# Kernel tuning notes

Measured on AMD Instinct MI355X. Metric: run time of the kernel, lower is better.

Reference implementation:

```python
import jax, jax.numpy as jnp
import numpy as np

EMBED = 1024
HEADS = 16
HEAD_DIM = EMBED // HEADS


def setup_inputs() -> dict:
    key = jax.random.key(0)
    ks = jax.random.split(key, 8)
    N, L = 2, 2048
    values = jax.random.normal(ks[0], (N, L, EMBED), dtype=jnp.float32)
    keys_ = jax.random.normal(ks[1], (N, L, EMBED), dtype=jnp.float32)
    query = jax.random.normal(ks[2], (N, L, EMBED), dtype=jnp.float32)
    mask = jnp.ones((N, 1, 1, L), dtype=jnp.int32)
    s = 1.0 / np.sqrt(EMBED)
    W_q = jax.random.normal(ks[3], (EMBED, EMBED), dtype=jnp.float32) * s
    W_k = jax.random.normal(ks[4], (EMBED, EMBED), dtype=jnp.float32) * s
    W_v = jax.random.normal(ks[5], (EMBED, EMBED), dtype=jnp.float32) * s
    W_o = jax.random.normal(ks[6], (EMBED, EMBED), dtype=jnp.float32) * s
    b_o = jax.random.normal(ks[7], (EMBED,), dtype=jnp.float32) * 0.01
    return {"values": values, "keys": keys_, "query": query, "mask": mask,
            "W_q": W_q, "W_k": W_k, "W_v": W_v, "W_o": W_o, "b_o": b_o}


def reference(values, keys, query, mask, W_q, W_k, W_v, W_o, b_o):
    N, Lq, _ = query.shape
    Lk = keys.shape[1]
    # projections (torch Linear: x @ W.T); reshape to (N, H, L, Dh)
    q = (query @ W_q.T).reshape(N, Lq, HEADS, HEAD_DIM).transpose(0, 2, 1, 3)
    k = (keys @ W_k.T).reshape(N, Lk, HEADS, HEAD_DIM).transpose(0, 2, 1, 3)
    v = (values @ W_v.T).reshape(N, Lk, HEADS, HEAD_DIM).transpose(0, 2, 1, 3)
    energy = jnp.einsum('bhqd,bhkd->bhqk', q, k) / jnp.sqrt(jnp.float32(HEAD_DIM))
    energy = jnp.where(mask == 0, jnp.float32(-1e20), energy)
    attn = jax.nn.softmax(energy, axis=-1)
    out = jnp.einsum('bhqk,bhkd->bhqd', attn, v)
    out = out.transpose(0, 2, 1, 3).reshape(N, Lq, EMBED)
    return out @ W_o.T + b_o
```

## Files before the change

### kernel.cpp

```cpp
#include <hip/hip_runtime.h>
#include <cstddef>
#include <cstdint>

#define SEQ    2048
#define NBATCH 2

typedef unsigned short u16;
typedef unsigned int   u32;
typedef __attribute__((ext_vector_type(8))) short bf16x8;
typedef __attribute__((ext_vector_type(4))) float f32x4;

#if __has_builtin(__builtin_amdgcn_exp2f)
#define EXP2F(x) __builtin_amdgcn_exp2f(x)
#else
#define EXP2F(x) exp2f(x)
#endif

__device__ __forceinline__ u32 fbits(float x) { union { float f; u32 u; } c; c.f = x; return c.u; }
__device__ __forceinline__ u16 f2bf(float x) { return (u16)((fbits(x) + 0x8000u) >> 16); }
__device__ __forceinline__ u32 pack2bf(float lo, float hi) {
    return __builtin_amdgcn_perm(fbits(hi) + 0x8000u, fbits(lo) + 0x8000u, 0x07060302u);
}

__global__ __launch_bounds__(256)
void cast_all(const float* __restrict__ q, const float* __restrict__ k, const float* __restrict__ v,
              const float* __restrict__ wq, const float* __restrict__ wk,
              const float* __restrict__ wv, const float* __restrict__ wo,
              u16* __restrict__ oq, u16* __restrict__ ok, u16* __restrict__ ov,
              u16* __restrict__ owq, u16* __restrict__ owk, u16* __restrict__ owv,
              u16* __restrict__ owo)
{
    const float* s; u16* d; int i;
    if (blockIdx.y == 0)      { s = q; d = oq; i = blockIdx.x * 256 + threadIdx.x; }
    else if (blockIdx.y == 1) { s = k; d = ok; i = blockIdx.x * 256 + threadIdx.x; }
    else if (blockIdx.y == 2) { s = v; d = ov; i = blockIdx.x * 256 + threadIdx.x; }
    else {
        const int w = blockIdx.x >> 10, xi = blockIdx.x & 1023;
        if (w == 0)      { s = wq; d = owq; }
        else if (w == 1) { s = wk; d = owk; }
        else if (w == 2) { s = wv; d = owv; }
        else             { s = wo; d = owo; }
        i = xi * 256 + threadIdx.x;
    }
    float4 vv = ((const float4*)s)[i];
    uint2 r; r.x = pack2bf(vv.x, vv.y); r.y = pack2bf(vv.z, vv.w);
    ((uint2*)d)[i] = r;
}

__device__ __forceinline__
void gemm_body(const u16* __restrict__ X, const u16* __restrict__ W,
               void* __restrict__ Yv, const int layout)
{
    __shared__ u16 smem[2 * 128 * 72];
    u16* As = smem;
    u16* Bs = smem + 128 * 72;

    const int tid  = threadIdx.x;
    const int wave = tid >> 6;
    const int lane = tid & 63;
    const int lm   = lane & 15;
    const int quad = lane >> 4;
    const int m0 = blockIdx.x * 128;
    const int n0 = blockIdx.y * 128;
    const int wr = (wave & 1) * 64;
    const int wc = (wave >> 1) * 64;

    const int srow = tid >> 1;
    const int scol = (tid & 1) * 32;
    const u16* xg = X + (size_t)(m0 + srow) * 1024 + scol;
    const u16* wg = W + (size_t)(n0 + srow) * 1024 + scol;

    bf16x8 pa[4], pb[4];
    #pragma unroll
    for (int p = 0; p < 4; ++p) {
        pa[p] = *(const bf16x8*)(xg + p * 8);
        pb[p] = *(const bf16x8*)(wg + p * 8);
    }

    f32x4 acc[4][4] = {};

    for (int k0 = 0; k0 < 1024; k0 += 64) {
        __syncthreads();
        #pragma unroll
        for (int p = 0; p < 4; ++p) {
            *(bf16x8*)&As[srow * 72 + scol + p * 8] = pa[p];
            *(bf16x8*)&Bs[srow * 72 + scol + p * 8] = pb[p];
        }
        __syncthreads();
        if (k0 + 64 < 1024) {
            #pragma unroll
            for (int p = 0; p < 4; ++p) {
                pa[p] = *(const bf16x8*)(xg + k0 + 64 + p * 8);
                pb[p] = *(const bf16x8*)(wg + k0 + 64 + p * 8);
            }
        }
        #pragma unroll
        for (int kk = 0; kk < 64; kk += 32) {
            bf16x8 af[4], bf[4];
            #pragma unroll
            for (int t = 0; t < 4; ++t) {
                af[t] = *(const bf16x8*)&As[(wr + t * 16 + lm) * 72 + kk + quad * 8];
                bf[t] = *(const bf16x8*)&Bs[(wc + t * 16 + lm) * 72 + kk + quad * 8];
            }
            #pragma unroll
            for (int i = 0; i < 4; ++i)
                #pragma unroll
                for (int j = 0; j < 4; ++j)
                    acc[i][j] = __builtin_amdgcn_mfma_f32_16x16x32_bf16(af[i], bf[j], acc[i][j], 0, 0, 0);
        }
    }

    if (layout == 0) {
        u16* Y = (u16*)Yv;
        #pragma unroll
        for (int i = 0; i < 4; ++i)
            #pragma unroll
            for (int j = 0; j < 4; ++j) {
                const int C = n0 + wc + j * 16 + lm;
                #pragma unroll
                for (int r = 0; r < 4; ++r) {
                    const int R = m0 + wr + i * 16 + quad * 4 + r;
                    Y[(size_t)R * 1024 + C] = f2bf(acc[i][j][r]);
                }
            }
    } else {
        __syncthreads();
        u16* T = smem;
        #pragma unroll
        for (int i = 0; i < 4; ++i)
            #pragma unroll
            for (int j = 0; j < 4; ++j) {
                const int col = wc + j * 16 + lm;
                const int row = wr + i * 16 + quad * 4;
                uint2 v;
                v.x = pack2bf(acc[i][j][0], acc[i][j][1]);
                v.y = pack2bf(acc[i][j][2], acc[i][j][3]);
                *(uint2*)&T[col * 132 + row] = v;
            }
        __syncthreads();
        const int dp = tid >> 1, half = (tid & 1) * 64;
        const int nn = m0 >> 11, l0 = m0 & 2047;
        const int C = n0 + dp, h = C >> 6, d = C & 63;
        u16* Y = (u16*)Yv;
        const size_t base = (((size_t)nn * 16 + h) * 64 + d) * SEQ + l0 + half;
        #pragma unroll
        for (int p = 0; p < 8; ++p) {
            bf16x8 v = *(const bf16x8*)&T[dp * 132 + half + p * 8];
            *(bf16x8*)(Y + base + p * 8) = v;
        }
    }
}

__global__ __launch_bounds__(256, 3)
void gemm_qkv(const u16* __restrict__ xq, const u16* __restrict__ xk, const u16* __restrict__ xv,
              const u16* __restrict__ wq, const u16* __restrict__ wk, const u16* __restrict__ wv,
              u16* __restrict__ qb, u16* __restrict__ kb, u16* __restrict__ vt)
{
    if (blockIdx.z == 0)      gemm_body(xq, wq, qb, 0);
    else if (blockIdx.z == 1) gemm_body(xk, wk, kb, 0);
    else                      gemm_body(xv, wv, vt, 2);
}

__global__ __launch_bounds__(256, 2)
void gemm_out64(const u16* __restrict__ X, const u16* __restrict__ W,
                float* __restrict__ Y, const float* __restrict__ bias)
{
    __shared__ u16 As[128 * 72];
    __shared__ u16 Bs[64 * 72];

    const int tid  = threadIdx.x;
    const int wave = tid >> 6;
    const int lane = tid & 63;
    const int lm   = lane & 15;
    const int quad = lane >> 4;
    const int m0 = blockIdx.x * 128;
    const int n0 = blockIdx.y * 64;
    const int wr = (wave & 1) * 64;
    const int wc = (wave >> 1) * 32;

    const int arow = tid >> 1, acol = (tid & 1) * 32;
    const int brow = tid >> 2, bcol = (tid & 3) * 16;
    const u16* xg = X + (size_t)(m0 + arow) * 1024 + acol;
    const u16* wg = W + (size_t)(n0 + brow) * 1024 + bcol;

    bf16x8 pa[4], pb[2];
    #pragma unroll
    for (int p = 0; p < 4; ++p) pa[p] = *(const bf16x8*)(xg + p * 8);
    #pragma unroll
    for (int p = 0; p < 2; ++p) pb[p] = *(const bf16x8*)(wg + p * 8);

    f32x4 acc[4][2] = {};

    for (int k0 = 0; k0 < 1024; k0 += 64) {
        __syncthreads();
        #pragma unroll
        for (int p = 0; p < 4; ++p) *(bf16x8*)&As[arow * 72 + acol + p * 8] = pa[p];
        #pragma unroll
        for (int p = 0; p < 2; ++p) *(bf16x8*)&Bs[brow * 72 + bcol + p * 8] = pb[p];
        __syncthreads();
        if (k0 + 64 < 1024) {
            #pragma unroll
            for (int p = 0; p < 4; ++p) pa[p] = *(const bf16x8*)(xg + k0 + 64 + p * 8);
            #pragma unroll
            for (int p = 0; p < 2; ++p) pb[p] = *(const bf16x8*)(wg + k0 + 64 + p * 8);
        }
        #pragma unroll
        for (int kk = 0; kk < 64; kk += 32) {
            bf16x8 af[4], bf[2];
            #pragma unroll
            for (int t = 0; t < 4; ++t)
                af[t] = *(const bf16x8*)&As[(wr + t * 16 + lm) * 72 + kk + quad * 8];
            #pragma unroll
            for (int j = 0; j < 2; ++j)
                bf[j] = *(const bf16x8*)&Bs[(wc + j * 16 + lm) * 72 + kk + quad * 8];
            #pragma unroll
            for (int i = 0; i < 4; ++i)
                #pragma unroll
                for (int j = 0; j < 2; ++j)
                    acc[i][j] = __builtin_amdgcn_mfma_f32_16x16x32_bf16(af[i], bf[j], acc[i][j], 0, 0, 0);
        }
    }

    #pragma unroll
    for (int i = 0; i < 4; ++i)
        #pragma unroll
        for (int j = 0; j < 2; ++j) {
            const int C = n0 + wc + j * 16 + lm;
            const float bv = bias[C];
            #pragma unroll
            for (int r = 0; r < 4; ++r) {
                const int R = m0 + wr + i * 16 + quad * 4 + r;
                Y[(size_t)R * 1024 + C] = acc[i][j][r] + bv;
            }
        }
}

__global__ __launch_bounds__(256, 2)
void flash_attn_bf16(const u16* __restrict__ Qb, const u16* __restrict__ Kb,
                     const u16* __restrict__ VT, const int* __restrict__ mask,
                     u16* __restrict__ O)
{
    __shared__ u16 Ks[128 * 72];
    __shared__ u16 Vts[64 * 136];
    __shared__ u16 Ps[4][32 * 72];

    const int tid  = threadIdx.x;
    const int wave = tid >> 6;
    const int lane = tid & 63;
    const int lm   = lane & 15;
    const int quad = lane >> 4;

    const int wid = blockIdx.x + 16 * blockIdx.y + 256 * blockIdx.z;
    const int idx = wid >> 3;
    const int hn  = (wid & 7) + 8 * (idx & 3);
    const int h   = hn & 15, n = hn >> 4;
    const int wq  = (idx >> 2) * 128 + wave * 32;

    const u16* Qh = Qb + ((size_t)n * SEQ) * 1024 + h * 64;
    const u16* Kh = Kb + ((size_t)n * SEQ) * 1024 + h * 64;
    const u16* Vh = VT + (((size_t)n * 16 + h) * 64) * SEQ;
    const int* mk = mask + (size_t)n * SEQ;
    u16* Pw = &Ps[wave][0];

    bf16x8 qf[2][2];
    #pragma unroll
    for (int t = 0; t < 2; ++t)
        #pragma unroll
        for (int s = 0; s < 2; ++s)
            qf[t][s] = *(const bf16x8*)(Qh + (size_t)(wq + t * 16 + lm) * 1024 + s * 32 + quad * 8);

    f32x4 o_acc[2][4] = {};
    float l_i[2][4] = {};

    const int kr = tid >> 1, kc = (tid & 1) * 32;
    const int vr = tid >> 2, vc = (tid & 3) * 32;

    bf16x8 ka[4], va[4];
    #pragma unroll
    for (int p = 0; p < 4; ++p) {
        ka[p] = *(const bf16x8*)(Kh + (size_t)kr * 1024 + kc + p * 8);
        va[p] = *(const bf16x8*)(Vh + (size_t)vr * SEQ + vc + p * 8);
    }

    const float cs = 0.125f * 1.44269504f;

    for (int c0 = 0; c0 < SEQ; c0 += 128) {
        __syncthreads();
        #pragma unroll
        for (int p = 0; p < 4; ++p) {
            *(bf16x8*)&Ks[kr * 72 + kc + p * 8]   = ka[p];
            *(bf16x8*)&Vts[vr * 136 + vc + p * 8] = va[p];
        }
        __syncthreads();

        if (c0 + 128 < SEQ) {
            #pragma unroll
            for (int p = 0; p < 4; ++p) {
                ka[p] = *(const bf16x8*)(Kh + (size_t)(c0 + 128 + kr) * 1024 + kc + p * 8);
                va[p] = *(const bf16x8*)(Vh + (size_t)vr * SEQ + c0 + 128 + vc + p * 8);
            }
        }

        f32x4 s[2][8] = {};
        #pragma unroll
        for (int nt = 0; nt < 8; ++nt) {
            bf16x8 kf0 = *(const bf16x8*)&Ks[(nt * 16 + lm) * 72 + quad * 8];
            bf16x8 kf1 = *(const bf16x8*)&Ks[(nt * 16 + lm) * 72 + 32 + quad * 8];
            #pragma unroll
            for (int t = 0; t < 2; ++t) {
                s[t][nt] = __builtin_amdgcn_mfma_f32_16x16x32_bf16(qf[t][0], kf0, s[t][nt], 0, 0, 0);
                s[t][nt] = __builtin_amdgcn_mfma_f32_16x16x32_bf16(qf[t][1], kf1, s[t][nt], 0, 0, 0);
            }
        }

        int msk[8];
        #pragma unroll
        for (int nt = 0; nt < 8; ++nt) msk[nt] = mk[c0 + nt * 16 + lm];
        #pragma unroll
        for (int t = 0; t < 2; ++t)
            #pragma unroll
            for (int nt = 0; nt < 8; ++nt)
                #pragma unroll
                for (int r = 0; r < 4; ++r) {
                    float e = EXP2F(s[t][nt][r] * cs);
                    e = msk[nt] ? e : 0.0f;
                    s[t][nt][r] = e;
                    l_i[t][r] += e;
                }

        #pragma unroll
        for (int half = 0; half < 2; ++half) {
            #pragma unroll
            for (int t = 0; t < 2; ++t)
                #pragma unroll
                for (int ntl = 0; ntl < 4; ++ntl)
                    #pragma unroll
                    for (int r = 0; r < 4; ++r)
                        Pw[(t * 16 + quad * 4 + r) * 72 + ntl * 16 + lm] =
                            f2bf(s[t][half * 4 + ntl][r]);

            #pragma unroll
            for (int ksl = 0; ksl < 2; ++ksl) {
                bf16x8 pf[2];
                #pragma unroll
                for (int t = 0; t < 2; ++t)
                    pf[t] = *(const bf16x8*)&Pw[(t * 16 + lm) * 72 + ksl * 32 + quad * 8];
                #pragma unroll
                for (int dt = 0; dt < 4; ++dt) {
                    bf16x8 vf = *(const bf16x8*)&Vts[(dt * 16 + lm) * 136 + half * 64 + ksl * 32 + quad * 8];
                    #pragma unroll
                    for (int t = 0; t < 2; ++t)
                        o_acc[t][dt] = __builtin_amdgcn_mfma_f32_16x16x32_bf16(pf[t], vf, o_acc[t][dt], 0, 0, 0);
                }
            }
        }
    }

    #pragma unroll
    for (int t = 0; t < 2; ++t)
        #pragma unroll
        for (int r = 0; r < 4; ++r) {
            float v = l_i[t][r];
            #pragma unroll
            for (int off = 1; off < 16; off <<= 1) v += __shfl_xor(v, off);
            l_i[t][r] = 1.0f / v;
        }
    #pragma unroll
    for (int t = 0; t < 2; ++t)
        #pragma unroll
        for (int dt = 0; dt < 4; ++dt)
            #pragma unroll
            for (int r = 0; r < 4; ++r) {
                const int ql = wq + t * 16 + quad * 4 + r;
                const int col = h * 64 + dt * 16 + lm;
                O[((size_t)n * SEQ + ql) * 1024 + col] = f2bf(o_acc[t][dt][r] * l_i[t][r]);
            }
}

extern "C" void kernel_launch(void* const* d_in, const int* in_sizes, int n_in,
                              void* d_out, int out_size, void* d_ws, size_t ws_size,
                              hipStream_t stream)
{
    const float* values = (const float*)d_in[0];
    const float* keys   = (const float*)d_in[1];
    const float* query  = (const float*)d_in[2];
    const int*   mask   = (const int*)d_in[3];
    const float* W_q    = (const float*)d_in[4];
    const float* W_k    = (const float*)d_in[5];
    const float* W_v    = (const float*)d_in[6];
    const float* W_o    = (const float*)d_in[7];
    const float* b_o    = (const float*)d_in[8];

    const size_t NTOK = (size_t)NBATCH * SEQ * 1024;
    const size_t WSZ  = 1024 * 1024;
    u16* p = (u16*)d_ws;
    u16* qb    = p; p += NTOK;
    u16* kb    = p; p += NTOK;
    u16* vt    = p; p += NTOK;
    u16* xq    = p; p += NTOK;
    u16* xk    = p; p += NTOK;
    u16* xv    = p; p += NTOK;
    u16* attnb = p; p += NTOK;
    u16* wqb   = p; p += WSZ;
    u16* wkb   = p; p += WSZ;
    u16* wvb   = p; p += WSZ;
    u16* wob   = p; p += WSZ;

    cast_all<<<dim3(4096, 4), 256, 0, stream>>>(query, keys, values,
                                                W_q, W_k, W_v, W_o,
                                                xq, xk, xv, wqb, wkb, wvb, wob);

    gemm_qkv<<<dim3(32, 8, 3), 256, 0, stream>>>(xq, xk, xv, wqb, wkb, wvb, qb, kb, vt);

    flash_attn_bf16<<<dim3(16, 16, 2), 256, 0, stream>>>(qb, kb, vt, mask, attnb);

    gemm_out64<<<dim3(32, 16), 256, 0, stream>>>(attnb, wob, (float*)d_out, b_o);
}
```

Measured before the change: 228.9 us.

## Split attention key range across blocks with atomic fp32 accumulation and combine pass

The flash attention kernel now splits the key sequence into two halves, doubling the block count to 1024. Each block accumulates its unnormalized output and row sums into zeroed fp32 buffers using atomicAdd. A new combine kernel then divides by the row sum and writes the bf16 attention output. Key tiles shrink to 64 and launch bounds rise to 4 blocks per CU, aiming for more parallelism and occupancy. The cost is a memset, atomic traffic on a 16MB fp32 buffer, and an extra elementwise pass.

New measurement: 244.3 us. 1.07x slower.

```diff
diff --git a/kernel.cpp b/kernel.cpp
--- a/kernel.cpp
+++ b/kernel.cpp
@@ -235,14 +235,14 @@
         }
 }
 
-__global__ __launch_bounds__(256, 2)
+__global__ __launch_bounds__(256, 4)
 void flash_attn_bf16(const u16* __restrict__ Qb, const u16* __restrict__ Kb,
                      const u16* __restrict__ VT, const int* __restrict__ mask,
-                     u16* __restrict__ O)
-{
-    __shared__ u16 Ks[128 * 72];
-    __shared__ u16 Vts[64 * 136];
-    __shared__ u16 Ps[4][32 * 72];
+                     float* __restrict__ O32, float* __restrict__ Lb)
+{
+    __shared__ u16 Ks[64 * 72];
+    __shared__ u16 Vts[64 * 72];
+    __shared__ u16 Ps[4][32 * 40];
 
     const int tid  = threadIdx.x;
     const int wave = tid >> 6;
@@ -250,11 +250,14 @@
     const int lm   = lane & 15;
     const int quad = lane >> 4;
 
-    const int wid = blockIdx.x + 16 * blockIdx.y + 256 * blockIdx.z;
-    const int idx = wid >> 3;
-    const int hn  = (wid & 7) + 8 * (idx & 3);
-    const int h   = hn & 15, n = hn >> 4;
-    const int wq  = (idx >> 2) * 128 + wave * 32;
+    const int wid  = blockIdx.x;
+    const int r_   = wid >> 3;
+    const int hn   = (wid & 7) + 8 * (r_ & 3);
+    const int h    = hn & 15, n = hn >> 4;
+    const int qblk = (r_ >> 2) & 15;
+    const int half = r_ >> 6;
+    const int wq   = qblk * 128 + wave * 32;
+    const int kbeg = half << 10;
 
     const u16* Qh = Qb + ((size_t)n * SEQ) * 1024 + h * 64;
     const u16* Kh = Kb + ((size_t)n * SEQ) * 1024 + h * 64;
@@ -272,38 +275,37 @@
     f32x4 o_acc[2][4] = {};
     float l_i[2][4] = {};
 
-    const int kr = tid >> 1, kc = (tid & 1) * 32;
-    const int vr = tid >> 2, vc = (tid & 3) * 32;
-
-    bf16x8 ka[4], va[4];
-    #pragma unroll
-    for (int p = 0; p < 4; ++p) {
-        ka[p] = *(const bf16x8*)(Kh + (size_t)kr * 1024 + kc + p * 8);
-        va[p] = *(const bf16x8*)(Vh + (size_t)vr * SEQ + vc + p * 8);
+    const int kr = tid >> 2, kc = (tid & 3) * 16;
+
+    bf16x8 ka[2], va[2];
+    #pragma unroll
+    for (int p = 0; p < 2; ++p) {
+        ka[p] = *(const bf16x8*)(Kh + (size_t)(kbeg + kr) * 1024 + kc + p * 8);
+        va[p] = *(const bf16x8*)(Vh + (size_t)kr * SEQ + kbeg + kc + p * 8);
     }
 
     const float cs = 0.125f * 1.44269504f;
 
-    for (int c0 = 0; c0 < SEQ; c0 += 128) {
-        __syncthreads();
-        #pragma unroll
-        for (int p = 0; p < 4; ++p) {
-            *(bf16x8*)&Ks[kr * 72 + kc + p * 8]   = ka[p];
-            *(bf16x8*)&Vts[vr * 136 + vc + p * 8] = va[p];
-        }
-        __syncthreads();
-
-        if (c0 + 128 < SEQ) {
-            #pragma unroll
-            for (int p = 0; p < 4; ++p) {
-                ka[p] = *(const bf16x8*)(Kh + (size_t)(c0 + 128 + kr) * 1024 + kc + p * 8);
-                va[p] = *(const bf16x8*)(Vh + (size_t)vr * SEQ + c0 + 128 + vc + p * 8);
-            }
-        }
-
-        f32x4 s[2][8] = {};
-        #pragma unroll
-        for (int nt = 0; nt < 8; ++nt) {
+    for (int c0 = kbeg; c0 < kbeg + 1024; c0 += 64) {
+        __syncthreads();
+        #pragma unroll
+        for (int p = 0; p < 2; ++p) {
+            *(bf16x8*)&Ks[kr * 72 + kc + p * 8]  = ka[p];
+            *(bf16x8*)&Vts[kr * 72 + kc + p * 8] = va[p];
+        }
+        __syncthreads();
+
+        if (c0 + 64 < kbeg + 1024) {
+            #pragma unroll
+            for (int p = 0; p < 2; ++p) {
+                ka[p] = *(const bf16x8*)(Kh + (size_t)(c0 + 64 + kr) * 1024 + kc + p * 8);
+                va[p] = *(const bf16x8*)(Vh + (size_t)kr * SEQ + c0 + 64 + kc + p * 8);
+            }
+        }
+
+        f32x4 s[2][4] = {};
+        #pragma unroll
+        for (int nt = 0; nt < 4; ++nt) {
             bf16x8 kf0 = *(const bf16x8*)&Ks[(nt * 16 + lm) * 72 + quad * 8];
             bf16x8 kf1 = *(const bf16x8*)&Ks[(nt * 16 + lm) * 72 + 32 + quad * 8];
             #pragma unroll
@@ -313,13 +315,13 @@
             }
         }
 
-        int msk[8];
-        #pragma unroll
-        for (int nt = 0; nt < 8; ++nt) msk[nt] = mk[c0 + nt * 16 + lm];
+        int msk[4];
+        #pragma unroll
+        for (int nt = 0; nt < 4; ++nt) msk[nt] = mk[c0 + nt * 16 + lm];
         #pragma unroll
         for (int t = 0; t < 2; ++t)
             #pragma unroll
-            for (int nt = 0; nt < 8; ++nt)
+            for (int nt = 0; nt < 4; ++nt)
                 #pragma unroll
                 for (int r = 0; r < 4; ++r) {
                     float e = EXP2F(s[t][nt][r] * cs);
@@ -329,29 +331,26 @@
                 }
 
         #pragma unroll
-        for (int half = 0; half < 2; ++half) {
+        for (int sb = 0; sb < 2; ++sb) {
             #pragma unroll
             for (int t = 0; t < 2; ++t)
                 #pragma unroll
-                for (int ntl = 0; ntl < 4; ++ntl)
+                for (int ntl = 0; ntl < 2; ++ntl)
                     #pragma unroll
                     for (int r = 0; r < 4; ++r)
-                        Pw[(t * 16 + quad * 4 + r) * 72 + ntl * 16 + lm] =
-                            f2bf(s[t][half * 4 + ntl][r]);
-
-            #pragma unroll
-            for (int ksl = 0; ksl < 2; ++ksl) {
-                bf16x8 pf[2];
+                        Pw[(t * 16 + quad * 4 + r) * 40 + ntl * 16 + lm] =
+                            f2bf(s[t][sb * 2 + ntl][r]);
+
+            bf16x8 pf[2];
+            #pragma unroll
+            for (int t = 0; t < 2; ++t)
+                pf[t] = *(const bf16x8*)&Pw[(t * 16 + lm) * 40 + quad * 8];
+            #pragma unroll
+            for (int dt = 0; dt < 4; ++dt) {
+                bf16x8 vf = *(const bf16x8*)&Vts[(dt * 16 + lm) * 72 + sb * 32 + quad * 8];
                 #pragma unroll
                 for (int t = 0; t < 2; ++t)
-                    pf[t] = *(const bf16x8*)&Pw[(t * 16 + lm) * 72 + ksl * 32 + quad * 8];
-                #pragma unroll
-                for (int dt = 0; dt < 4; ++dt) {
-                    bf16x8 vf = *(const bf16x8*)&Vts[(dt * 16 + lm) * 136 + half * 64 + ksl * 32 + quad * 8];
-                    #pragma unroll
-                    for (int t = 0; t < 2; ++t)
-                        o_acc[t][dt] = __builtin_amdgcn_mfma_f32_16x16x32_bf16(pf[t], vf, o_acc[t][dt], 0, 0, 0);
-                }
+                    o_acc[t][dt] = __builtin_amdgcn_mfma_f32_16x16x32_bf16(pf[t], vf, o_acc[t][dt], 0, 0, 0);
             }
         }
     }
@@ -363,8 +362,17 @@
             float v = l_i[t][r];
             #pragma unroll
             for (int off = 1; off < 16; off <<= 1) v += __shfl_xor(v, off);
-            l_i[t][r] = 1.0f / v;
-        }
+            l_i[t][r] = v;
+        }
+    if (lm == 0) {
+        #pragma unroll
+        for (int t = 0; t < 2; ++t)
+            #pragma unroll
+            for (int r = 0; r < 4; ++r) {
+                const int ql = wq + t * 16 + quad * 4 + r;
+                atomicAdd(&Lb[(((size_t)n * 16 + h) << 11) + ql], l_i[t][r]);
+            }
+    }
     #pragma unroll
     for (int t = 0; t < 2; ++t)
         #pragma unroll
@@ -373,8 +381,23 @@
             for (int r = 0; r < 4; ++r) {
                 const int ql = wq + t * 16 + quad * 4 + r;
                 const int col = h * 64 + dt * 16 + lm;
-                O[((size_t)n * SEQ + ql) * 1024 + col] = f2bf(o_acc[t][dt][r] * l_i[t][r]);
-            }
+                atomicAdd(&O32[(((size_t)n * SEQ + ql) << 10) + col], o_acc[t][dt][r]);
+            }
+}
+
+__global__ __launch_bounds__(256)
+void combine_norm(const float* __restrict__ O32, const float* __restrict__ Lb,
+                  u16* __restrict__ attnb)
+{
+    const int i = blockIdx.x * 256 + threadIdx.x;
+    float4 o = ((const float4*)O32)[i];
+    const int e4 = i & 255;
+    const int h  = e4 >> 4;
+    const int l  = (i >> 8) & 2047;
+    const int n  = i >> 19;
+    const float inv = 1.0f / Lb[(((size_t)n * 16 + h) << 11) + l];
+    uint2 r; r.x = pack2bf(o.x * inv, o.y * inv); r.y = pack2bf(o.z * inv, o.w * inv);
+    ((uint2*)attnb)[i] = r;
 }
 
 extern "C" void kernel_launch(void* const* d_in, const int* in_sizes, int n_in,
@@ -405,6 +428,8 @@
     u16* wkb   = p; p += WSZ;
     u16* wvb   = p; p += WSZ;
     u16* wob   = p; p += WSZ;
+    float* O32 = (float*)xq;
+    float* Lb  = (float*)xv;
 
     cast_all<<<dim3(4096, 4), 256, 0, stream>>>(query, keys, values,
                                                 W_q, W_k, W_v, W_o,
@@ -412,7 +437,11 @@
 
     gemm_qkv<<<dim3(32, 8, 3), 256, 0, stream>>>(xq, xk, xv, wqb, wkb, wvb, qb, kb, vt);
 
-    flash_attn_bf16<<<dim3(16, 16, 2), 256, 0, stream>>>(qb, kb, vt, mask, attnb);
+    hipMemsetAsync(O32, 0, NTOK * 4 + 65536 * 4, stream);
+
+    flash_attn_bf16<<<1024, 256, 0, stream>>>(qb, kb, vt, mask, O32, Lb);
+
+    combine_norm<<<4096, 256, 0, stream>>>(O32, Lb, attnb);
 
     gemm_out64<<<dim3(32, 16), 256, 0, stream>>>(attnb, wob, (float*)d_out, b_o);
 }
```

## Load GEMM tiles directly into LDS with global_load_lds, drop register prefetch

Applied to the files above, without the earlier changes.

Both projection GEMMs now move tiles from global memory straight into shared memory using the direct global-to-LDS load builtin, replacing the register-staged double-buffer prefetch. LDS rows lose their padding (stride 72 becomes 64) to fit the builtin's contiguous per-wave layout. This removes VGPR staging and the ds_write instructions, but it also drops the overlap of the next tile's load with the current MFMAs. The unpadded layout may also cause LDS bank conflicts on the fragment reads.

Result: no change. 229.7 us (+0.3%).

```diff
diff --git a/kernel.cpp b/kernel.cpp
--- a/kernel.cpp
+++ b/kernel.cpp
@@ -15,6 +15,10 @@
 #else
 #define EXP2F(x) exp2f(x)
 #endif
+
+#define GLL16(g, l) __builtin_amdgcn_global_load_lds( \
+    (const __attribute__((address_space(1))) void*)(g), \
+    (__attribute__((address_space(3))) void*)(l), 16, 0, 0)
 
 __device__ __forceinline__ u32 fbits(float x) { union { float f; u32 u; } c; c.f = x; return c.u; }
 __device__ __forceinline__ u16 f2bf(float x) { return (u16)((fbits(x) + 0x8000u) >> 16); }
@@ -51,9 +55,9 @@
 void gemm_body(const u16* __restrict__ X, const u16* __restrict__ W,
                void* __restrict__ Yv, const int layout)
 {
-    __shared__ u16 smem[2 * 128 * 72];
+    __shared__ u16 smem[16896];
     u16* As = smem;
-    u16* Bs = smem + 128 * 72;
+    u16* Bs = smem + 8192;
 
     const int tid  = threadIdx.x;
     const int wave = tid >> 6;
@@ -65,42 +69,28 @@
     const int wr = (wave & 1) * 64;
     const int wc = (wave >> 1) * 64;
 
-    const int srow = tid >> 1;
-    const int scol = (tid & 1) * 32;
+    const int srow = wave * 32 + (lane >> 3);
+    const int scol = (lane & 7) * 8;
     const u16* xg = X + (size_t)(m0 + srow) * 1024 + scol;
     const u16* wg = W + (size_t)(n0 + srow) * 1024 + scol;
 
-    bf16x8 pa[4], pb[4];
-    #pragma unroll
-    for (int p = 0; p < 4; ++p) {
-        pa[p] = *(const bf16x8*)(xg + p * 8);
-        pb[p] = *(const bf16x8*)(wg + p * 8);
-    }
-
     f32x4 acc[4][4] = {};
 
     for (int k0 = 0; k0 < 1024; k0 += 64) {
         __syncthreads();
         #pragma unroll
         for (int p = 0; p < 4; ++p) {
-            *(bf16x8*)&As[srow * 72 + scol + p * 8] = pa[p];
-            *(bf16x8*)&Bs[srow * 72 + scol + p * 8] = pb[p];
-        }
-        __syncthreads();
-        if (k0 + 64 < 1024) {
-            #pragma unroll
-            for (int p = 0; p < 4; ++p) {
-                pa[p] = *(const bf16x8*)(xg + k0 + 64 + p * 8);
-                pb[p] = *(const bf16x8*)(wg + k0 + 64 + p * 8);
-            }
-        }
+            GLL16(xg + k0 + p * 8 * 1024, &As[(wave * 32 + p * 8) * 64]);
+            GLL16(wg + k0 + p * 8 * 1024, &Bs[(wave * 32 + p * 8) * 64]);
+        }
+        __syncthreads();
         #pragma unroll
         for (int kk = 0; kk < 64; kk += 32) {
             bf16x8 af[4], bf[4];
             #pragma unroll
             for (int t = 0; t < 4; ++t) {
-                af[t] = *(const bf16x8*)&As[(wr + t * 16 + lm) * 72 + kk + quad * 8];
-                bf[t] = *(const bf16x8*)&Bs[(wc + t * 16 + lm) * 72 + kk + quad * 8];
+                af[t] = *(const bf16x8*)&As[(wr + t * 16 + lm) * 64 + kk + quad * 8];
+                bf[t] = *(const bf16x8*)&Bs[(wc + t * 16 + lm) * 64 + kk + quad * 8];
             }
             #pragma unroll
             for (int i = 0; i < 4; ++i)
@@ -165,8 +155,8 @@
 void gemm_out64(const u16* __restrict__ X, const u16* __restrict__ W,
                 float* __restrict__ Y, const float* __restrict__ bias)
 {
-    __shared__ u16 As[128 * 72];
-    __shared__ u16 Bs[64 * 72];
+    __shared__ u16 As[128 * 64];
+    __shared__ u16 Bs[64 * 64];
 
     const int tid  = threadIdx.x;
     const int wave = tid >> 6;
@@ -178,41 +168,30 @@
     const int wr = (wave & 1) * 64;
     const int wc = (wave >> 1) * 32;
 
-    const int arow = tid >> 1, acol = (tid & 1) * 32;
-    const int brow = tid >> 2, bcol = (tid & 3) * 16;
-    const u16* xg = X + (size_t)(m0 + arow) * 1024 + acol;
-    const u16* wg = W + (size_t)(n0 + brow) * 1024 + bcol;
-
-    bf16x8 pa[4], pb[2];
-    #pragma unroll
-    for (int p = 0; p < 4; ++p) pa[p] = *(const bf16x8*)(xg + p * 8);
-    #pragma unroll
-    for (int p = 0; p < 2; ++p) pb[p] = *(const bf16x8*)(wg + p * 8);
+    const int sr8 = lane >> 3, sc8 = (lane & 7) * 8;
+    const u16* xg = X + (size_t)(m0 + wave * 32 + sr8) * 1024 + sc8;
+    const u16* wg = W + (size_t)(n0 + wave * 16 + sr8) * 1024 + sc8;
 
     f32x4 acc[4][2] = {};
 
     for (int k0 = 0; k0 < 1024; k0 += 64) {
         __syncthreads();
         #pragma unroll
-        for (int p = 0; p < 4; ++p) *(bf16x8*)&As[arow * 72 + acol + p * 8] = pa[p];
-        #pragma unroll
-        for (int p = 0; p < 2; ++p) *(bf16x8*)&Bs[brow * 72 + bcol + p * 8] = pb[p];
-        __syncthreads();
-        if (k0 + 64 < 1024) {
-            #pragma unroll
-            for (int p = 0; p < 4; ++p) pa[p] = *(const bf16x8*)(xg + k0 + 64 + p * 8);
-            #pragma unroll
-            for (int p = 0; p < 2; ++p) pb[p] = *(const bf16x8*)(wg + k0 + 64 + p * 8);
-        }
+        for (int p = 0; p < 4; ++p)
+            GLL16(xg + k0 + p * 8 * 1024, &As[(wave * 32 + p * 8) * 64]);
+        #pragma unroll
+        for (int p = 0; p < 2; ++p)
+            GLL16(wg + k0 + p * 8 * 1024, &Bs[(wave * 16 + p * 8) * 64]);
+        __syncthreads();
         #pragma unroll
         for (int kk = 0; kk < 64; kk += 32) {
             bf16x8 af[4], bf[2];
             #pragma unroll
             for (int t = 0; t < 4; ++t)
-                af[t] = *(const bf16x8*)&As[(wr + t * 16 + lm) * 72 + kk + quad * 8];
+                af[t] = *(const bf16x8*)&As[(wr + t * 16 + lm) * 64 + kk + quad * 8];
             #pragma unroll
             for (int j = 0; j < 2; ++j)
-                bf[j] = *(const bf16x8*)&Bs[(wc + j * 16 + lm) * 72 + kk + quad * 8];
+                bf[j] = *(const bf16x8*)&Bs[(wc + j * 16 + lm) * 64 + kk + quad * 8];
             #pragma unroll
             for (int i = 0; i < 4; ++i)
                 #pragma unroll
```
